# Kernel tuning notes

Measured on AMD Instinct MI355X. Metric: run time of the kernel, lower is better.

Reference implementation:

```python
import jax, jax.numpy as jnp
import numpy as np
import math

D_MODEL = 512

def setup_inputs() -> dict:
    key = jax.random.key(0)
    k1, k2, k3 = jax.random.split(key, 3)
    X = jax.random.normal(k1, (4, 8192, D_MODEL), dtype=jnp.float32)
    # nn.Linear(d, d, bias=False) weights, applied as x @ W.T
    s = 1.0 / math.sqrt(D_MODEL)
    W_v = jax.random.uniform(k2, (D_MODEL, D_MODEL), dtype=jnp.float32, minval=-s, maxval=s)
    W_theta = jax.random.uniform(k3, (D_MODEL, D_MODEL), dtype=jnp.float32, minval=-s, maxval=s)
    return {"X": X, "W_v": W_v, "W_theta": W_theta}

def reference(X, W_v, W_theta):
    # X: [B, n, d]
    n = X.shape[1]
    d = X.shape[2]
    XW_v = X @ W_v.T            # [B, n, d]
    theta_X = X @ W_theta.T     # [B, n, d]
    # first term: (1/n) * ones(n,n) @ XW_v == column mean broadcast over rows
    first_term = jnp.mean(XW_v, axis=1, keepdims=True)  # [B, 1, d], broadcasts
    # second term: (1/(n*sqrt(d))) * (X @ theta_X^T) @ XW_v
    # associativity-reduced: theta_X^T @ XW_v is [B, d, d]
    kv = jnp.einsum('bnd,bne->bde', theta_X, XW_v)       # [B, d, d]
    second_term = (X @ kv) / (n * math.sqrt(d))          # [B, n, d]
    return first_term + second_term
```

## Files before the change

kernel.cpp:

```cpp
#include <hip/hip_runtime.h>
#include <stdint.h>


typedef __bf16 bf16x8 __attribute__((ext_vector_type(8)));
typedef float f32x4 __attribute__((ext_vector_type(4)));
typedef unsigned short u16x4 __attribute__((ext_vector_type(4)));
typedef unsigned short u16x8 __attribute__((ext_vector_type(8)));

#define BK 32

#define BAR asm volatile("s_barrier" ::: "memory")

template <int N>
__device__ __forceinline__ void vmw() {
  static_assert(N == 0 || N == 1 || N == 2 || N == 4 || N == 8, "vmw");
  if constexpr (N == 0) asm volatile("s_waitcnt vmcnt(0)" ::: "memory");
  else if constexpr (N == 1) asm volatile("s_waitcnt vmcnt(1)" ::: "memory");
  else if constexpr (N == 2) asm volatile("s_waitcnt vmcnt(2)" ::: "memory");
  else if constexpr (N == 4) asm volatile("s_waitcnt vmcnt(4)" ::: "memory");
  else if constexpr (N == 8) asm volatile("s_waitcnt vmcnt(8)" ::: "memory");
}

__device__ __forceinline__ unsigned short f2bf(float f) {
  union { float f; unsigned int u; } c; c.f = f;
  unsigned int u = c.u;
  return (unsigned short)((u + 0x7FFFu + ((u >> 16) & 1u)) >> 16);
}
__device__ __forceinline__ float bf2f(unsigned short h) {
  union { unsigned int u; float f; } c; c.u = ((unsigned int)h) << 16;
  return c.f;
}

__device__ __forceinline__ void gld16(const void* g, void* l) {
  using gptr_t = const __attribute__((address_space(1))) void*;
  using lptr_t = __attribute__((address_space(3))) void*;
  __builtin_amdgcn_global_load_lds((gptr_t)(uintptr_t)g,
                                   (lptr_t)(uint32_t)(uintptr_t)l, 16, 0, 0);
}

template <int TB, bool SAME>
__device__ __forceinline__ void gemm_tile(const unsigned short* __restrict__ A, int lda,
                                          const unsigned short* __restrict__ B, int ldb,
                                          int m0, int n0, f32x4 (&acc)[TB / 32][TB / 32]) {
  static_assert(TB == 64 || TB == 128, "TB");
  constexpr int FR = TB / 32;
  constexpr int LJ = (TB * 4) / 256;
  constexpr int LPS = SAME ? LJ : 2 * LJ;
  constexpr int NK = 512 / BK;
  __shared__ unsigned short sA[3][TB * BK];
  __shared__ unsigned short sB[3][TB * BK];
  const int tid = threadIdx.x;
  const int lane = tid & 63;
  const int w = tid >> 6;
  const int wm = w >> 1, wn = w & 1;
  const int quad = lane >> 4, l16 = lane & 15;
  const int sq = (quad ^ ((l16 >> 1) & 3)) * 8;

#pragma unroll
  for (int mi = 0; mi < FR; mi++)
#pragma unroll
    for (int ni = 0; ni < FR; ni++) acc[mi][ni] = f32x4{0.f, 0.f, 0.f, 0.f};

  auto stage = [&](int bb, int kt) {
    const int kk = kt * BK;
#pragma unroll
    for (int j = 0; j < LJ; j++) {
      const int slot = w * (LJ * 64) + j * 64 + lane;
      const int row = slot >> 2;
      const int col = ((slot & 3) ^ ((slot >> 3) & 3)) * 8;
      const int basegr = w * (LJ * 64) + j * 64;
      gld16(A + (size_t)(m0 + row) * lda + kk + col, (char*)sA[bb] + (size_t)basegr * 16);
      if constexpr (!SAME)
        gld16(B + (size_t)(n0 + row) * ldb + kk + col, (char*)sB[bb] + (size_t)basegr * 16);
    }
  };

  auto compute = [&](int bb) {
    const unsigned short* as = sA[bb];
    const unsigned short* bs = SAME ? sA[bb] : sB[bb];
    bf16x8 af[FR], bfr[FR];
#pragma unroll
    for (int mi = 0; mi < FR; mi++)
      af[mi] = *(const bf16x8*)&as[(wm * (TB / 2) + mi * 16 + l16) * BK + sq];
#pragma unroll
    for (int ni = 0; ni < FR; ni++)
      bfr[ni] = *(const bf16x8*)&bs[(wn * (TB / 2) + ni * 16 + l16) * BK + sq];
    __builtin_amdgcn_s_setprio(1);
#pragma unroll
    for (int mi = 0; mi < FR; mi++)
#pragma unroll
      for (int ni = 0; ni < FR; ni++)
        acc[mi][ni] = __builtin_amdgcn_mfma_f32_16x16x32_bf16(af[mi], bfr[ni],
                                                              acc[mi][ni], 0, 0, 0);
    __builtin_amdgcn_s_setprio(0);
  };

  stage(0, 0);
  stage(1, 1);
  stage(2, 2);
#pragma unroll
  for (int kt = 0; kt < NK; ++kt) {
    if (kt < NK - 2) { vmw<2 * LPS>(); }
    else if (kt == NK - 2) { vmw<LPS>(); }
    else { vmw<0>(); }
    BAR;
    compute(kt % 3);
    BAR;
    if (kt < NK - 3) stage(kt % 3, kt + 3);
  }
}

__global__ __launch_bounds__(256) void prep_kernel(const float* __restrict__ X,
                                                   unsigned short* __restrict__ Xb,
                                                   unsigned short* __restrict__ Xt,
                                                   float* __restrict__ mean_x) {
  __shared__ unsigned short sw[4][64 * 32];
  const int t = threadIdx.x;
  const int w = t >> 6, l = t & 63;
  const int g = blockIdx.x * 4 + w;
  const int d0 = (g & 15) * 32;
  const int n64 = (g >> 4) * 64;
  const int b = n64 >> 13, nb = n64 & 8191;
  const int a = l >> 3, q = l & 7;
  const int c0 = q * 4;
  unsigned short* myw = sw[w];

  f32x4 v[8];
#pragma unroll
  for (int i = 0; i < 8; i++)
    v[i] = *(const f32x4*)(X + (size_t)(n64 + a + 8 * i) * 512 + d0 + c0);
  __builtin_amdgcn_sched_barrier(0);

  u16x4 o[8];
#pragma unroll
  for (int i = 0; i < 8; i++)
#pragma unroll
    for (int j = 0; j < 4; j++) o[i][j] = f2bf(v[i][j]);

#pragma unroll
  for (int j = 0; j < 4; j++) {
    u16x8 wv;
#pragma unroll
    for (int i = 0; i < 8; i++) wv[i] = o[i][j];
    const int c = c0 + j;
    const int pos = a ^ ((c >> 2) & 7);
    *(u16x8*)&myw[c * 64 + pos * 8] = wv;
  }

#pragma unroll
  for (int i = 0; i < 8; i++)
    *(u16x4*)(Xb + (size_t)(n64 + a + 8 * i) * 512 + d0 + c0) = o[i];

  asm volatile("s_waitcnt lgkmcnt(0)" ::: "memory");

  float cs[4];
#pragma unroll
  for (int h = 0; h < 4; h++) {
    const int cp = a + 8 * h;
    const int pos = q ^ ((cp >> 2) & 7);
    u16x8 val = *(const u16x8*)&myw[cp * 64 + pos * 8];
    *(u16x8*)(Xt + (size_t)(b * 512 + d0 + cp) * 8192 + nb + q * 8) = val;
    float ss = 0.f;
#pragma unroll
    for (int jj = 0; jj < 8; jj++) ss += bf2f(val[jj]);
    cs[h] = ss;
  }
#pragma unroll
  for (int h = 0; h < 4; h++) {
    float sv = cs[h];
    sv += __shfl_xor(sv, 1);
    sv += __shfl_xor(sv, 2);
    sv += __shfl_xor(sv, 4);
    if (q == 0) atomicAdd(&mean_x[b * 512 + d0 + a + 8 * h], sv);
  }
}

__global__ __launch_bounds__(256) void prep_w_kernel(const float* __restrict__ Wv,
                                                     const float* __restrict__ Wth,
                                                     unsigned short* __restrict__ Wvb,
                                                     unsigned short* __restrict__ Wtb,
                                                     float* __restrict__ mean_x) {
  const int blk = blockIdx.x;
  const int t = threadIdx.x;
  if (blk == 0) {
#pragma unroll
    for (int i = 0; i < 8; i++) mean_x[t + i * 256] = 0.f;
  }
  const float* src = (blk < 128) ? Wv : Wth;
  unsigned short* dst = (blk < 128) ? Wvb : Wtb;
  const int i = (blk & 127) * 256 + t;
  const f32x4* pp = (const f32x4*)(src + (size_t)i * 8);
  f32x4 v0 = pp[0], v1 = pp[1];
  u16x8 o;
  o[0] = f2bf(v0[0]); o[1] = f2bf(v0[1]); o[2] = f2bf(v0[2]); o[3] = f2bf(v0[3]);
  o[4] = f2bf(v1[0]); o[5] = f2bf(v1[1]); o[6] = f2bf(v1[2]); o[7] = f2bf(v1[3]);
  *(u16x8*)(dst + (size_t)i * 8) = o;
}

static __device__ const int TI[10] = {0, 0, 0, 0, 1, 1, 1, 2, 2, 3};
static __device__ const int TJ[10] = {0, 1, 2, 3, 1, 2, 3, 2, 3, 3};

__global__ __launch_bounds__(256) void g_gemm_kernel(const unsigned short* __restrict__ Xt,
                                                     float* __restrict__ G_part) {
  const int t = blockIdx.y;
  const int z = blockIdx.x;
  const int b = z >> 4, s = z & 15;
  const int m0 = TI[t] * 128, n0 = TJ[t] * 128;
  const unsigned short* A = Xt + (size_t)b * 512 * 8192 + (size_t)s * 512;
  f32x4 acc[4][4];
  if (m0 == n0)
    gemm_tile<128, true>(A, 8192, A, 8192, m0, n0, acc);
  else
    gemm_tile<128, false>(A, 8192, A, 8192, m0, n0, acc);
  float* Cp = G_part + ((size_t)z * 10 + t) * 16384;
  const int tid = threadIdx.x, lane = tid & 63, w = tid >> 6;
  const int wm = w >> 1, wn = w & 1, quad = lane >> 4, l16 = lane & 15;
#pragma unroll
  for (int mi = 0; mi < 4; mi++)
#pragma unroll
    for (int ni = 0; ni < 4; ni++) {
      const int ml = wm * 64 + mi * 16 + quad * 4;
      const int nl = wn * 64 + ni * 16 + l16;
      *(f32x4*)(Cp + (size_t)nl * 128 + ml) = acc[mi][ni];
    }
}

__global__ __launch_bounds__(256) void g_fin_kernel(const float* __restrict__ G_part,
                                                    unsigned short* __restrict__ Gb,
                                                    const float* __restrict__ mean_x,
                                                    const float* __restrict__ Wv,
                                                    float* __restrict__ meanV) {
  const int blk = blockIdx.x;
  if (blk >= 320) {
    const int idx = (blk - 320) * 256 + threadIdx.x;
    const int b = idx >> 9, e = idx & 511;
    const float* mx = mean_x + b * 512;
    const float* wr = Wv + (size_t)e * 512;
    float s = 0.f;
    for (int d = 0; d < 512; d += 4) {
      f32x4 a = *(const f32x4*)(mx + d);
      f32x4 w4 = *(const f32x4*)(wr + d);
      s += a[0] * w4[0] + a[1] * w4[1] + a[2] * w4[2] + a[3] * w4[3];
    }
    meanV[idx] = s * (1.f / 8192.f);
    return;
  }
  const int b = blk / 80, rem = blk % 80;
  const int t = rem >> 3, cc = rem & 7;
  const int i = TI[t], j = TJ[t];
  const int m0 = i * 128, n0 = j * 128;
  const int tid = threadIdx.x;
  const int np = cc * 16 + (tid >> 4);
  const int mp = (tid & 15) * 8;
  f32x4 s0 = f32x4{0.f, 0.f, 0.f, 0.f}, s1 = f32x4{0.f, 0.f, 0.f, 0.f};
#pragma unroll
  for (int s = 0; s < 16; s++) {
    const float* p = G_part + (((size_t)(b * 16 + s)) * 10 + t) * 16384 + (size_t)np * 128 + mp;
    s0 += *(const f32x4*)p;
    s1 += *(const f32x4*)(p + 4);
  }
  const float scale = (float)(1.0 / (8192.0 * 22.627416997969522));
  unsigned short h[8];
#pragma unroll
  for (int r = 0; r < 4; r++) { h[r] = f2bf(s0[r] * scale); h[r + 4] = f2bf(s1[r] * scale); }
  unsigned short* Gbb = Gb + (size_t)b * 262144;
#pragma unroll
  for (int r = 0; r < 8; r++)
    Gbb[(size_t)(m0 + mp + r) * 512 + (n0 + np)] = h[r];
  if (i != j) {
    u16x8 o;
#pragma unroll
    for (int r = 0; r < 8; r++) o[r] = h[r];
    *(u16x8*)(Gbb + (size_t)(n0 + np) * 512 + (m0 + mp)) = o;
  }
}

__global__ __launch_bounds__(256) void gemm_rm_kernel(const unsigned short* __restrict__ A,
                                                      const unsigned short* __restrict__ B,
                                                      unsigned short* __restrict__ C,
                                                      size_t Abs, size_t Bbs) {
  const int b = blockIdx.z;
  const int m0 = blockIdx.x * 64, n0 = blockIdx.y * 64;
  f32x4 acc[2][2];
  gemm_tile<64, false>(A + (size_t)b * Abs, 512, B + (size_t)b * Bbs, 512, m0, n0, acc);
  unsigned short* Cb = C + (size_t)b * 262144;
  const int tid = threadIdx.x, lane = tid & 63, w = tid >> 6;
  const int wm = w >> 1, wn = w & 1, quad = lane >> 4, l16 = lane & 15;
#pragma unroll
  for (int mi = 0; mi < 2; mi++)
#pragma unroll
    for (int ni = 0; ni < 2; ni++) {
      const int m = m0 + wm * 32 + mi * 16 + quad * 4;
      const int n = n0 + wn * 32 + ni * 16 + l16;
#pragma unroll
      for (int r = 0; r < 4; r++)
        Cb[(size_t)(m + r) * 512 + n] = f2bf(acc[mi][ni][r]);
    }
}

__global__ __launch_bounds__(256) void gemm_out_kernel(
    const unsigned short* __restrict__ Xb, const unsigned short* __restrict__ kvt,
    const float* __restrict__ meanV, float* __restrict__ out) {
  const int D = blockIdx.x;
  const int gm = (D & 7) + ((D >> 5) << 3);
  const int nt = (D >> 3) & 3;
  const int m0 = gm * 128, n0 = nt * 128;
  const int b = gm >> 6;
  const unsigned short* Bm = kvt + (size_t)b * 262144;
  f32x4 acc[4][4];
  gemm_tile<128, false>(Xb, 512, Bm, 512, m0, n0, acc);
  const int tid = threadIdx.x, lane = tid & 63, w = tid >> 6;
  const int wm = w >> 1, wn = w & 1, quad = lane >> 4, l16 = lane & 15;
#pragma unroll
  for (int ni = 0; ni < 4; ni++) {
    const int e = n0 + wn * 64 + ni * 16 + l16;
    const float mu = meanV[b * 512 + e];
#pragma unroll
    for (int mi = 0; mi < 4; mi++) {
      const int m = m0 + wm * 64 + mi * 16 + quad * 4;
#pragma unroll
      for (int r = 0; r < 4; r++)
        out[(size_t)(m + r) * 512 + e] = acc[mi][ni][r] + mu;
    }
  }
}

extern "C" void kernel_launch(void* const* d_in, const int* in_sizes, int n_in,
                              void* d_out, int out_size, void* d_ws, size_t ws_size,
                              hipStream_t stream) {
  const float* X = (const float*)d_in[0];
  const float* Wv = (const float*)d_in[1];
  const float* Wth = (const float*)d_in[2];
  float* out = (float*)d_out;
  char* ws = (char*)d_ws;

  unsigned short* Xb = (unsigned short*)(ws);
  unsigned short* Xt = (unsigned short*)(ws + 33554432ull);
  float* G_part = (float*)(ws + 67108864ull);
  unsigned short* Gb = (unsigned short*)(ws + 109051904ull);
  unsigned short* Ht = (unsigned short*)(ws + 111149056ull);
  unsigned short* kvt = (unsigned short*)(ws + 113246208ull);
  unsigned short* Wvb = (unsigned short*)(ws + 115343360ull);
  unsigned short* Wtb = (unsigned short*)(ws + 115867648ull);
  float* mean_x = (float*)(ws + 116391936ull);
  float* meanV = (float*)(ws + 116400128ull);

  prep_w_kernel<<<256, 256, 0, stream>>>(Wv, Wth, Wvb, Wtb, mean_x);
  prep_kernel<<<2048, 256, 0, stream>>>(X, Xb, Xt, mean_x);

  g_gemm_kernel<<<dim3(64, 10), 256, 0, stream>>>(Xt, G_part);
  g_fin_kernel<<<328, 256, 0, stream>>>(G_part, Gb, mean_x, Wv, meanV);

  gemm_rm_kernel<<<dim3(8, 8, 4), 256, 0, stream>>>(Wvb, Gb, Ht, 0, 262144);
  gemm_rm_kernel<<<dim3(8, 8, 4), 256, 0, stream>>>(Ht, Wtb, kvt, 262144, 0);

  gemm_out_kernel<<<1024, 256, 0, stream>>>(Xb, kvt, meanV, out);
}
```

Before: 216.1 us.

## Drop transposed X copy; compute Gram GEMM from row-major X with transpose LDS reads

The prep kernel no longer writes a transposed bf16 copy of X. The Gram-matrix GEMM now loads row-major Xb tiles and uses ds_read_b64_tr_b16 transpose reads from LDS to build MFMA operands. This removes a 32 MB global write plus the LDS transpose in prep, and prep is restructured into larger blocks that reduce column sums with fewer atomics. The trade-offs are a new GEMM tile path whose LDS layout and bank-conflict behaviour are untested, and strided row loads in the GEMM.

```diff
diff --git a/kernel.cpp b/kernel.cpp
--- a/kernel.cpp
+++ b/kernel.cpp
@@ -6,6 +6,7 @@
 typedef float f32x4 __attribute__((ext_vector_type(4)));
 typedef unsigned short u16x4 __attribute__((ext_vector_type(4)));
 typedef unsigned short u16x8 __attribute__((ext_vector_type(8)));
+typedef unsigned int u32x2 __attribute__((ext_vector_type(2)));
 
 #define BK 32
 
@@ -110,68 +111,142 @@
   }
 }
 
+template <bool SAME>
+__device__ __forceinline__ void gemm_tile_nt(const unsigned short* __restrict__ Xs,
+                                             int m0, int n0, f32x4 (&acc)[4][4]) {
+  constexpr int LPS = SAME ? 2 : 4;
+  constexpr int NK = 16;
+  __shared__ unsigned short sA[3][128 * BK];
+  __shared__ unsigned short sB[3][128 * BK];
+  const int tid = threadIdx.x;
+  const int lane = tid & 63;
+  const int w = tid >> 6;
+  const int wm = w >> 1, wn = w & 1;
+  const int quad = lane >> 4, l16 = lane & 15;
+
+#pragma unroll
+  for (int mi = 0; mi < 4; mi++)
+#pragma unroll
+    for (int ni = 0; ni < 4; ni++) acc[mi][ni] = f32x4{0.f, 0.f, 0.f, 0.f};
+
+  auto stage = [&](int bb, int kt) {
+#pragma unroll
+    for (int j = 0; j < 2; j++) {
+      const int g = w * 128 + j * 64 + lane;
+      const int dblk = g >> 6;
+      const int nblk = (g >> 3) & 7;
+      const int nr = (g >> 1) & 3;
+      const int half = g & 1;
+      const int n = kt * 32 + nblk * 4 + nr;
+      const int base = w * 128 + j * 64;
+      gld16(Xs + (size_t)n * 512 + m0 + dblk * 16 + half * 8,
+            (char*)sA[bb] + (size_t)base * 16);
+      if constexpr (!SAME)
+        gld16(Xs + (size_t)n * 512 + n0 + dblk * 16 + half * 8,
+              (char*)sB[bb] + (size_t)base * 16);
+    }
+  };
+
+  auto compute = [&](int bb) {
+    const unsigned int abase =
+        (unsigned int)(uintptr_t)(&sA[bb][0]) + (unsigned int)(quad * 256 + l16 * 8);
+    const unsigned int bbase =
+        (SAME ? (unsigned int)(uintptr_t)(&sA[bb][0])
+              : (unsigned int)(uintptr_t)(&sB[bb][0])) +
+        (unsigned int)(quad * 256 + l16 * 8);
+    u32x2 ra[4][2], rb[4][2];
+#pragma unroll
+    for (int mi = 0; mi < 4; mi++) {
+      const unsigned int pa = abase + (unsigned int)((wm * 4 + mi) * 1024);
+      asm volatile("ds_read_b64_tr_b16 %0, %1" : "=v"(ra[mi][0]) : "v"(pa));
+      asm volatile("ds_read_b64_tr_b16 %0, %1 offset:128" : "=v"(ra[mi][1]) : "v"(pa));
+    }
+#pragma unroll
+    for (int ni = 0; ni < 4; ni++) {
+      const unsigned int pb = bbase + (unsigned int)((wn * 4 + ni) * 1024);
+      asm volatile("ds_read_b64_tr_b16 %0, %1" : "=v"(rb[ni][0]) : "v"(pb));
+      asm volatile("ds_read_b64_tr_b16 %0, %1 offset:128" : "=v"(rb[ni][1]) : "v"(pb));
+    }
+    asm volatile("s_waitcnt lgkmcnt(0)" ::: "memory");
+    __builtin_amdgcn_sched_barrier(0);
+    union U { unsigned int u[4]; bf16x8 v; };
+    bf16x8 af[4], bfr[4];
+#pragma unroll
+    for (int mi = 0; mi < 4; mi++) {
+      U ua;
+      ua.u[0] = ra[mi][0][0]; ua.u[1] = ra[mi][0][1];
+      ua.u[2] = ra[mi][1][0]; ua.u[3] = ra[mi][1][1];
+      af[mi] = ua.v;
+    }
+#pragma unroll
+    for (int ni = 0; ni < 4; ni++) {
+      U ub;
+      ub.u[0] = rb[ni][0][0]; ub.u[1] = rb[ni][0][1];
+      ub.u[2] = rb[ni][1][0]; ub.u[3] = rb[ni][1][1];
+      bfr[ni] = ub.v;
+    }
+    __builtin_amdgcn_s_setprio(1);
+#pragma unroll
+    for (int mi = 0; mi < 4; mi++)
+#pragma unroll
+      for (int ni = 0; ni < 4; ni++)
+        acc[mi][ni] = __builtin_amdgcn_mfma_f32_16x16x32_bf16(af[mi], bfr[ni],
+                                                              acc[mi][ni], 0, 0, 0);
+    __builtin_amdgcn_s_setprio(0);
+  };
+
+  stage(0, 0);
+  stage(1, 1);
+  stage(2, 2);
+#pragma unroll
+  for (int kt = 0; kt < NK; ++kt) {
+    if (kt < NK - 2) { vmw<2 * LPS>(); }
+    else if (kt == NK - 2) { vmw<LPS>(); }
+    else { vmw<0>(); }
+    BAR;
+    compute(kt % 3);
+    BAR;
+    if (kt < NK - 3) stage(kt % 3, kt + 3);
+  }
+}
+
 __global__ __launch_bounds__(256) void prep_kernel(const float* __restrict__ X,
                                                    unsigned short* __restrict__ Xb,
-                                                   unsigned short* __restrict__ Xt,
                                                    float* __restrict__ mean_x) {
-  __shared__ unsigned short sw[4][64 * 32];
   const int t = threadIdx.x;
-  const int w = t >> 6, l = t & 63;
-  const int g = blockIdx.x * 4 + w;
-  const int d0 = (g & 15) * 32;
-  const int n64 = (g >> 4) * 64;
-  const int b = n64 >> 13, nb = n64 & 8191;
-  const int a = l >> 3, q = l & 7;
-  const int c0 = q * 4;
-  unsigned short* myw = sw[w];
-
-  f32x4 v[8];
-#pragma unroll
-  for (int i = 0; i < 8; i++)
-    v[i] = *(const f32x4*)(X + (size_t)(n64 + a + 8 * i) * 512 + d0 + c0);
-  __builtin_amdgcn_sched_barrier(0);
-
-  u16x4 o[8];
-#pragma unroll
-  for (int i = 0; i < 8; i++)
-#pragma unroll
-    for (int j = 0; j < 4; j++) o[i][j] = f2bf(v[i][j]);
-
+  const int bid = blockIdx.x;
+  const int n0 = (bid >> 3) * 256;
+  const int d0 = (bid & 7) * 64;
+  const int b = n0 >> 13;
+  const int rg = t >> 4;
+  const int c = t & 15;
+  float cs[4] = {0.f, 0.f, 0.f, 0.f};
+#pragma unroll
+  for (int hb = 0; hb < 2; hb++) {
+    f32x4 v[8];
+#pragma unroll
+    for (int i = 0; i < 8; i++) {
+      const int r = rg + 16 * (hb * 8 + i);
+      v[i] = *(const f32x4*)(X + (size_t)(n0 + r) * 512 + d0 + c * 4);
+    }
+    __builtin_amdgcn_sched_barrier(0);
+#pragma unroll
+    for (int i = 0; i < 8; i++) {
+      const int r = rg + 16 * (hb * 8 + i);
+      u16x4 o;
+#pragma unroll
+      for (int j = 0; j < 4; j++) o[j] = f2bf(v[i][j]);
+      *(u16x4*)(Xb + (size_t)(n0 + r) * 512 + d0 + c * 4) = o;
+#pragma unroll
+      for (int j = 0; j < 4; j++) cs[j] += bf2f(o[j]);
+    }
+  }
 #pragma unroll
   for (int j = 0; j < 4; j++) {
-    u16x8 wv;
-#pragma unroll
-    for (int i = 0; i < 8; i++) wv[i] = o[i][j];
-    const int c = c0 + j;
-    const int pos = a ^ ((c >> 2) & 7);
-    *(u16x8*)&myw[c * 64 + pos * 8] = wv;
-  }
-
-#pragma unroll
-  for (int i = 0; i < 8; i++)
-    *(u16x4*)(Xb + (size_t)(n64 + a + 8 * i) * 512 + d0 + c0) = o[i];
-
-  asm volatile("s_waitcnt lgkmcnt(0)" ::: "memory");
-
-  float cs[4];
-#pragma unroll
-  for (int h = 0; h < 4; h++) {
-    const int cp = a + 8 * h;
-    const int pos = q ^ ((cp >> 2) & 7);
-    u16x8 val = *(const u16x8*)&myw[cp * 64 + pos * 8];
-    *(u16x8*)(Xt + (size_t)(b * 512 + d0 + cp) * 8192 + nb + q * 8) = val;
-    float ss = 0.f;
-#pragma unroll
-    for (int jj = 0; jj < 8; jj++) ss += bf2f(val[jj]);
-    cs[h] = ss;
-  }
-#pragma unroll
-  for (int h = 0; h < 4; h++) {
-    float sv = cs[h];
-    sv += __shfl_xor(sv, 1);
-    sv += __shfl_xor(sv, 2);
-    sv += __shfl_xor(sv, 4);
-    if (q == 0) atomicAdd(&mean_x[b * 512 + d0 + a + 8 * h], sv);
+    float sv = cs[j];
+    sv += __shfl_xor(sv, 16);
+    sv += __shfl_xor(sv, 32);
+    if ((t & 63) < 16) atomicAdd(&mean_x[b * 512 + d0 + c * 4 + j], sv);
   }
 }
 
@@ -200,18 +275,18 @@
 static __device__ const int TI[10] = {0, 0, 0, 0, 1, 1, 1, 2, 2, 3};
 static __device__ const int TJ[10] = {0, 1, 2, 3, 1, 2, 3, 2, 3, 3};
 
-__global__ __launch_bounds__(256) void g_gemm_kernel(const unsigned short* __restrict__ Xt,
+__global__ __launch_bounds__(256) void g_gemm_kernel(const unsigned short* __restrict__ Xb,
                                                      float* __restrict__ G_part) {
   const int t = blockIdx.y;
   const int z = blockIdx.x;
   const int b = z >> 4, s = z & 15;
   const int m0 = TI[t] * 128, n0 = TJ[t] * 128;
-  const unsigned short* A = Xt + (size_t)b * 512 * 8192 + (size_t)s * 512;
+  const unsigned short* Xs = Xb + (size_t)(b * 8192 + s * 512) * 512;
   f32x4 acc[4][4];
   if (m0 == n0)
-    gemm_tile<128, true>(A, 8192, A, 8192, m0, n0, acc);
+    gemm_tile_nt<true>(Xs, m0, n0, acc);
   else
-    gemm_tile<128, false>(A, 8192, A, 8192, m0, n0, acc);
+    gemm_tile_nt<false>(Xs, m0, n0, acc);
   float* Cp = G_part + ((size_t)z * 10 + t) * 16384;
   const int tid = threadIdx.x, lane = tid & 63, w = tid >> 6;
   const int wm = w >> 1, wn = w & 1, quad = lane >> 4, l16 = lane & 15;
@@ -335,7 +410,6 @@
   char* ws = (char*)d_ws;
 
   unsigned short* Xb = (unsigned short*)(ws);
-  unsigned short* Xt = (unsigned short*)(ws + 33554432ull);
   float* G_part = (float*)(ws + 67108864ull);
   unsigned short* Gb = (unsigned short*)(ws + 109051904ull);
   unsigned short* Ht = (unsigned short*)(ws + 111149056ull);
@@ -346,9 +420,9 @@
   float* meanV = (float*)(ws + 116400128ull);
 
   prep_w_kernel<<<256, 256, 0, stream>>>(Wv, Wth, Wvb, Wtb, mean_x);
-  prep_kernel<<<2048, 256, 0, stream>>>(X, Xb, Xt, mean_x);
-
-  g_gemm_kernel<<<dim3(64, 10), 256, 0, stream>>>(Xt, G_part);
+  prep_kernel<<<1024, 256, 0, stream>>>(X, Xb, mean_x);
+
+  g_gemm_kernel<<<dim3(64, 10), 256, 0, stream>>>(Xb, G_part);
   g_fin_kernel<<<328, 256, 0, stream>>>(G_part, Gb, mean_x, Wv, meanV);
 
   gemm_rm_kernel<<<dim3(8, 8, 4), 256, 0, stream>>>(Wvb, Gb, Ht, 0, 262144);
```

Result: slower. 226.2 us (+4.7%).
